# Optimization experiments

Measured on AMD Instinct MI355X. Metric: run time of the kernel, lower is better.

Reference implementation:

```python
import jax, jax.numpy as jnp
import numpy as np

N = 50000        # nodes
E = 1600000      # edges
NFEAT = 128      # node feature dim
NEDGE = 16       # raw edge feature dim
NHID = 128
NLAYER = 4
NGRAPH = 512
NOUT = 128
BN_EPS = 1e-5


def _bn(h, g, b):
    # eval-mode BatchNorm1d with running_mean=0, running_var=1
    return h * (g / jnp.sqrt(1.0 + BN_EPS)) + b


def setup_inputs() -> dict:
    key = jax.random.key(0)
    ks = jax.random.split(key, 24)
    s = 0.05
    inp = {
        "x": jax.random.normal(ks[0], (N, NFEAT), jnp.float32),
        "edge_index": jax.random.randint(ks[1], (2, E), 0, N, jnp.int64),
        "edge_attr": jax.random.normal(ks[2], (E, NEDGE), jnp.float32),
        "batch": jnp.sort(jax.random.randint(ks[3], (N,), 0, NGRAPH, jnp.int64)),
        # input encoder MLP (Linear + BN + ReLU)
        "in_W": jax.random.normal(ks[4], (NFEAT, NHID), jnp.float32) * s,
        "in_b": jnp.zeros((NHID,), jnp.float32),
        "in_g": jnp.ones((NHID,), jnp.float32),
        "in_beta": jnp.zeros((NHID,), jnp.float32),
        # per-layer edge encoder MLPs
        "edge_W": jax.random.normal(ks[5], (NLAYER, NEDGE, NHID), jnp.float32) * s,
        "edge_b": jnp.zeros((NLAYER, NHID), jnp.float32),
        "edge_g": jnp.ones((NLAYER, NHID), jnp.float32),
        "edge_beta": jnp.zeros((NLAYER, NHID), jnp.float32),
        # per-layer GINEConv linear (bias=False since bn=True) and eps
        "conv_W": jax.random.normal(ks[6], (NLAYER, NHID, NHID), jnp.float32) * s,
        "eps": jnp.zeros((NLAYER,), jnp.float32),
        # per-layer BatchNorm after conv
        "bn_g": jnp.ones((NLAYER, NHID), jnp.float32),
        "bn_b": jnp.zeros((NLAYER, NHID), jnp.float32),
        # output encoder: 2-layer MLP, norm after layer 1, no final activation
        "out_W1": jax.random.normal(ks[7], (NHID, NHID), jnp.float32) * s,
        "out_b1": jnp.zeros((NHID,), jnp.float32),
        "out_g1": jnp.ones((NHID,), jnp.float32),
        "out_beta1": jnp.zeros((NHID,), jnp.float32),
        "out_W2": jax.random.normal(ks[8], (NHID, NOUT), jnp.float32) * s,
        "out_b2": jnp.zeros((NOUT,), jnp.float32),
    }
    return inp


def reference(x, edge_index, edge_attr, batch,
              in_W, in_b, in_g, in_beta,
              edge_W, edge_b, edge_g, edge_beta,
              conv_W, eps, bn_g, bn_b,
              out_W1, out_b1, out_g1, out_beta1,
              out_W2, out_b2):
    # input encoder (MLP, 1 layer: Linear + BN + ReLU)
    h = jax.nn.relu(_bn(x @ in_W + in_b, in_g, in_beta))
    prev = h
    src, dst = edge_index[0], edge_index[1]
    for l in range(NLAYER):
        # edge encoder
        ea = jax.nn.relu(_bn(edge_attr @ edge_W[l] + edge_b[l], edge_g[l], edge_beta[l]))
        # GINEConv: messages relu(x_src + e), sum-aggregate to dst
        m = jax.nn.relu(h[src] + ea)                         # [E, NHID]
        agg = jax.ops.segment_sum(m, dst, num_segments=N)    # [N, NHID]
        h = ((1.0 + eps[l]) * h + agg) @ conv_W[l]
        h = jax.nn.relu(_bn(h, bn_g[l], bn_b[l]))            # dropout=0
        h = h + prev                                         # residual
        prev = h
    # add pooling over graphs
    pooled = jax.ops.segment_sum(h, batch, num_segments=NGRAPH)  # [NGRAPH, NHID]
    # output encoder: Linear+BN+ReLU, then Linear
    o = jax.nn.relu(_bn(pooled @ out_W1 + out_b1, out_g1, out_beta1))
    return o @ out_W2 + out_b2
```

## Files before the change

kernel.cpp:

```cpp
#include <hip/hip_runtime.h>
#include <stdint.h>

typedef uint32_t u32;
typedef _Float16 h2v __attribute__((ext_vector_type(2)));
typedef __attribute__((ext_vector_type(8))) short bf16x8;
typedef __attribute__((ext_vector_type(4))) float f32x4;

#define NGRAPH 512

__device__ __forceinline__ float uif(u32 u) { return __builtin_bit_cast(float, u); }
__device__ __forceinline__ u32 fiu(float f) { return __builtin_bit_cast(u32, f); }
__device__ __forceinline__ unsigned short bf16r(float f) {
    return (unsigned short)((fiu(f) + 0x8000u) >> 16);
}
__device__ __forceinline__ u32 pack_bf16(float lo, float hi) {
    return ((fiu(lo) + 0x8000u) >> 16) | ((fiu(hi) + 0x8000u) & 0xFFFF0000u);
}
__device__ __forceinline__ u32 pkh(float a, float b) {
    unsigned short la = __builtin_bit_cast(unsigned short, (_Float16)a);
    unsigned short hb = __builtin_bit_cast(unsigned short, (_Float16)b);
    return (u32)la | ((u32)hb << 16);
}
__device__ __forceinline__ float fdot2w(u32 a, u32 b, float c) {
#if __has_builtin(__builtin_amdgcn_fdot2)
    return __builtin_amdgcn_fdot2(__builtin_bit_cast(h2v, a),
                                  __builtin_bit_cast(h2v, b), c, false);
#else
    h2v av = __builtin_bit_cast(h2v, a), bv = __builtin_bit_cast(h2v, b);
    return c + (float)av[0]*(float)bv[0] + (float)av[1]*(float)bv[1];
#endif
}

__global__ __launch_bounds__(256) void prep_kernel(
    const float* __restrict__ in_b, const float* __restrict__ in_g, const float* __restrict__ in_beta,
    const float* __restrict__ edge_W,
    const float* __restrict__ edge_b, const float* __restrict__ edge_g, const float* __restrict__ edge_beta,
    const float* __restrict__ bn_g, const float* __restrict__ bn_b,
    const float* __restrict__ out_b1, const float* __restrict__ out_g1, const float* __restrict__ out_beta1,
    float* __restrict__ consts, u32* __restrict__ wpk)
{
    int c = threadIdx.x;
    if (c >= 128) return;
    const float rs = rsqrtf(1.0f + 1e-5f);
    float es = in_g[c] * rs;
    consts[c]       = es;
    consts[128 + c] = in_b[c] * es + in_beta[c];
    for (int l = 0; l < 4; ++l) {
        float s = edge_g[l*128 + c] * rs;
        consts[256  + l*128 + c] = s;
        consts[768  + l*128 + c] = edge_b[l*128 + c] * s + edge_beta[l*128 + c];
        float bs = bn_g[l*128 + c] * rs;
        consts[1280 + l*128 + c] = bs;
        consts[1792 + l*128 + c] = bn_b[l*128 + c];
        for (int kk = 0; kk < 8; ++kk) {
            float w0 = edge_W[(l*16 + 2*kk)*128 + c];
            float w1 = edge_W[(l*16 + 2*kk + 1)*128 + c];
            wpk[(l*8 + kk)*128 + c] = pkh(w0, w1);
        }
    }
    float s1 = out_g1[c] * rs;
    consts[2304 + c] = s1;
    consts[2432 + c] = out_b1[c] * s1 + out_beta1[c];
}

__global__ __launch_bounds__(256) void prepw_kernel(
    const float* __restrict__ in_W, const float* __restrict__ conv_W,
    unsigned short* __restrict__ WtAll)
{
    for (int idx = blockIdx.x*blockDim.x + threadIdx.x; idx < 5*128*128;
         idx += gridDim.x*blockDim.x) {
        int w = idx >> 14, rem = idx & 16383;
        int nn = rem >> 7, kk = rem & 127;
        const float* S = (w == 0) ? in_W : conv_W + (size_t)(w-1)*16384;
        WtAll[idx] = bf16r(S[kk*128 + nn]);
    }
}

__global__ __launch_bounds__(256) void xconv_kernel(
    const float* __restrict__ x, u32* __restrict__ x16, int n4)
{
    for (int i = blockIdx.x*blockDim.x + threadIdx.x; i < n4;
         i += gridDim.x*blockDim.x) {
        float4 v = *(const float4*)(x + (size_t)i*4);
        uint2 o; o.x = pack_bf16(v.x, v.y); o.y = pack_bf16(v.z, v.w);
        *(uint2*)(x16 + (size_t)i*2) = o;
    }
}

__global__ __launch_bounds__(256) void count_kernel(
    const int* __restrict__ dst, int E, int* __restrict__ cnt)
{
    for (int e = blockIdx.x*blockDim.x + threadIdx.x; e < E; e += gridDim.x*blockDim.x)
        atomicAdd(&cnt[dst[e]], 1);
}

__global__ __launch_bounds__(1024) void scan_kernel(
    const int* __restrict__ cnt, int n, int E,
    int* __restrict__ offs, int* __restrict__ cursor)
{
    __shared__ int sh[1024];
    const int t = threadIdx.x;
    const int chunk = (n + 1023) >> 10;
    const int lo = t * chunk;
    const int hi = min(n, lo + chunk);
    int s = 0;
    for (int i = lo; i < hi; ++i) s += cnt[i];
    sh[t] = s;
    __syncthreads();
    for (int d = 1; d < 1024; d <<= 1) {
        int v = (t >= d) ? sh[t - d] : 0;
        __syncthreads();
        sh[t] += v;
        __syncthreads();
    }
    int base = sh[t] - s;
    for (int i = lo; i < hi; ++i) { int c = cnt[i]; offs[i] = base; cursor[i] = base; base += c; }
    if (t == 1023) offs[n] = E;
}

__global__ __launch_bounds__(256) void scatter_kernel(
    const int* __restrict__ src, const int* __restrict__ dst,
    const float* __restrict__ attr, int E,
    int* __restrict__ cursor, int* __restrict__ srcoff, uint4* __restrict__ attrp)
{
    for (int e = blockIdx.x*blockDim.x + threadIdx.x; e < E; e += gridDim.x*blockDim.x) {
        int p = atomicAdd(&cursor[dst[e]], 1);
        srcoff[p] = src[e] * 256;
        const float4* ar = (const float4*)(attr + (size_t)e*16);
        float4 v0 = ar[0], v1 = ar[1], v2 = ar[2], v3 = ar[3];
        uint4 o0, o1;
        o0.x = pkh(v0.x, v0.y); o0.y = pkh(v0.z, v0.w);
        o0.z = pkh(v1.x, v1.y); o0.w = pkh(v1.z, v1.w);
        o1.x = pkh(v2.x, v2.y); o1.y = pkh(v2.z, v2.w);
        o1.z = pkh(v3.x, v3.y); o1.w = pkh(v3.z, v3.w);
        attrp[2*(size_t)p] = o0; attrp[2*(size_t)p + 1] = o1;
    }
}

__global__ __launch_bounds__(256) void goff_kernel(
    const int* __restrict__ batch, int n, int* __restrict__ goff)
{
    int g = blockIdx.x*blockDim.x + threadIdx.x;
    if (g > NGRAPH) return;
    if (g == NGRAPH) { goff[NGRAPH] = n; return; }
    int lo = 0, hi = n;
    while (lo < hi) { int m = (lo + hi) >> 1; if (batch[m] < g) lo = m + 1; else hi = m; }
    goff[g] = lo;
}

__global__ __launch_bounds__(256) void conv_mfma_kernel(
    const unsigned short* X16, int M,
    const unsigned short* __restrict__ Wt,
    const float* __restrict__ scale, const float* __restrict__ off,
    const unsigned short* __restrict__ resid16,
    unsigned short* out16, int do_relu)
{
    __shared__ unsigned short Ws[128*128];
    for (int i = threadIdx.x*8; i < 128*128; i += 256*8) {
        int row = i >> 7;
        int bo = (i & 127) * 2;
        int4 v = *(const int4*)(Wt + i);
        *(int4*)((char*)Ws + row*256 + (bo ^ ((row & 7) << 4))) = v;
    }
    __syncthreads();
    const int wave = threadIdx.x >> 6, lane = threadIdx.x & 63;
    const int row0 = blockIdx.x*64 + wave*16;
    const int l15 = lane & 15, l4 = lane >> 4;
    int arow = row0 + l15; if (arow > M-1) arow = M-1;
    const unsigned short* ap = X16 + (size_t)arow*128 + l4*8;
    f32x4 acc[8];
    #pragma unroll
    for (int t = 0; t < 8; ++t) acc[t] = f32x4{0.f, 0.f, 0.f, 0.f};
    #pragma unroll
    for (int ks = 0; ks < 4; ++ks) {
        bf16x8 a = *(const bf16x8*)(ap + ks*32);
        #pragma unroll
        for (int t = 0; t < 8; ++t) {
            int brow = t*16 + l15;
            int bo = ks*64 + l4*16;
            bf16x8 b = *(const bf16x8*)((const char*)Ws + brow*256 + (bo ^ ((brow & 7) << 4)));
            acc[t] = __builtin_amdgcn_mfma_f32_16x16x32_bf16(a, b, acc[t], 0, 0, 0);
        }
    }
    #pragma unroll
    for (int t = 0; t < 8; ++t) {
        int col = t*16 + l15;
        float sc = scale[col], of = off[col];
        #pragma unroll
        for (int r = 0; r < 4; ++r) {
            int row = row0 + l4*4 + r;
            if (row < M) {
                float y = fmaf(acc[t][r], sc, of);
                if (do_relu) y = fmaxf(y, 0.f);
                if (resid16) y += uif((u32)resid16[(size_t)row*128 + col] << 16);
                out16[(size_t)row*128 + col] = bf16r(y);
            }
        }
    }
}

__global__ __launch_bounds__(256) void agg_kernel(
    const char* __restrict__ hb,
    const uint4* __restrict__ attrp,
    const int* __restrict__ srcoff,
    const int* __restrict__ offs,
    const u32* __restrict__ wpk,
    const float* __restrict__ escale, const float* __restrict__ eoff,
    const float* __restrict__ epsp, int layer,
    u32* __restrict__ C16, int n)
{
    const int wave = threadIdx.x >> 6, lane = threadIdx.x & 63;
    const int lane4 = lane * 4;
    const int c0 = lane * 2;
    u32 wA[8], wB[8];
    #pragma unroll
    for (int kk = 0; kk < 8; ++kk) {
        wA[kk] = wpk[(layer*8 + kk)*128 + c0];
        wB[kk] = wpk[(layer*8 + kk)*128 + c0 + 1];
    }
    const float sc0 = escale[c0], sc1 = escale[c0+1];
    const float of0 = eoff[c0],   of1 = eoff[c0+1];
    const float epsv = 1.0f + epsp[layer];

    for (int node = blockIdx.x*4 + wave; node < n; node += gridDim.x*4) {
        const int beg = offs[node], end = offs[node+1];
        float acc0 = 0.f, acc1 = 0.f;

        auto edge = [&](int idx) {
            const int iu = __builtin_amdgcn_readfirstlane(idx);
            const uint4 q0 = attrp[2*(size_t)iu];
            const uint4 q1 = attrp[2*(size_t)iu + 1];
            const int so = srcoff[iu];
            const u32 hv = *(const u32*)(hb + so + lane4);
            float r0 = 0.f, r1 = 0.f;
            r0 = fdot2w(q0.x, wA[0], r0); r1 = fdot2w(q0.x, wB[0], r1);
            r0 = fdot2w(q0.y, wA[1], r0); r1 = fdot2w(q0.y, wB[1], r1);
            r0 = fdot2w(q0.z, wA[2], r0); r1 = fdot2w(q0.z, wB[2], r1);
            r0 = fdot2w(q0.w, wA[3], r0); r1 = fdot2w(q0.w, wB[3], r1);
            r0 = fdot2w(q1.x, wA[4], r0); r1 = fdot2w(q1.x, wB[4], r1);
            r0 = fdot2w(q1.y, wA[5], r0); r1 = fdot2w(q1.y, wB[5], r1);
            r0 = fdot2w(q1.z, wA[6], r0); r1 = fdot2w(q1.z, wB[6], r1);
            r0 = fdot2w(q1.w, wA[7], r0); r1 = fdot2w(q1.w, wB[7], r1);
            float ea0 = fmaxf(fmaf(r0, sc0, of0), 0.f);
            float ea1 = fmaxf(fmaf(r1, sc1, of1), 0.f);
            float h0 = uif(hv << 16);
            float h1 = uif(hv & 0xFFFF0000u);
            acc0 += fmaxf(h0 + ea0, 0.f);
            acc1 += fmaxf(h1 + ea1, 0.f);
        };

        int i = beg;
        for (; i + 1 < end; i += 2) { edge(i); edge(i + 1); }
        if (i < end) edge(i);

        const u32 hn = *(const u32*)(hb + (size_t)node*256 + lane4);
        float t0 = fmaf(epsv, uif(hn << 16), acc0);
        float t1 = fmaf(epsv, uif(hn & 0xFFFF0000u), acc1);
        C16[(size_t)node*64 + lane] = pack_bf16(t0, t1);
    }
}

__global__ __launch_bounds__(256) void pool_kernel(
    const u32* __restrict__ h16, const int* __restrict__ goff,
    float* __restrict__ pooled)
{
    const int wave = threadIdx.x >> 6, lane = threadIdx.x & 63;
    const int g = blockIdx.x*4 + wave;
    if (g >= NGRAPH) return;
    float ax = 0.f, ay = 0.f;
    const int beg = goff[g], end = goff[g+1];
    for (int node = beg; node < end; ++node) {
        u32 v = h16[(size_t)node*64 + lane];
        ax += uif(v << 16); ay += uif(v & 0xFFFF0000u);
    }
    *(float2*)&pooled[g*128 + lane*2] = make_float2(ax, ay);
}

__global__ __launch_bounds__(256) void gemm128_kernel(
    const float* __restrict__ in, int rows,
    const float* __restrict__ W,
    const float* __restrict__ scale, const float* __restrict__ off,
    float* out, int do_relu)
{
    __shared__ float Wsh[128*128];
    for (int i = threadIdx.x*4; i < 128*128; i += 256*4)
        *(float4*)&Wsh[i] = *(const float4*)&W[i];
    __syncthreads();
    const int wave = threadIdx.x >> 6, lane = threadIdx.x & 63;
    const int c0 = lane * 2;
    const float sc0 = scale ? scale[c0]   : 1.0f;
    const float sc1 = scale ? scale[c0+1] : 1.0f;
    const float of0 = off ? off[c0]   : 0.0f;
    const float of1 = off ? off[c0+1] : 0.0f;
    for (int rp = blockIdx.x*4 + wave; rp*2 < rows; rp += gridDim.x*4) {
        const int row0 = __builtin_amdgcn_readfirstlane(rp * 2);
        const float* xr = in + (size_t)row0 * 128;
        float a00 = 0.f, a01 = 0.f, a10 = 0.f, a11 = 0.f;
        #pragma unroll 8
        for (int k = 0; k < 128; ++k) {
            float x0 = xr[k];
            float x1 = xr[128 + k];
            float2 w = *(const float2*)&Wsh[k*128 + c0];
            a00 = fmaf(x0, w.x, a00); a01 = fmaf(x0, w.y, a01);
            a10 = fmaf(x1, w.x, a10); a11 = fmaf(x1, w.y, a11);
        }
        float y00 = fmaf(a00, sc0, of0), y01 = fmaf(a01, sc1, of1);
        float y10 = fmaf(a10, sc0, of0), y11 = fmaf(a11, sc1, of1);
        if (do_relu) {
            y00 = fmaxf(y00, 0.f); y01 = fmaxf(y01, 0.f);
            y10 = fmaxf(y10, 0.f); y11 = fmaxf(y11, 0.f);
        }
        *(float2*)&out[(size_t)row0*128 + c0]     = make_float2(y00, y01);
        *(float2*)&out[(size_t)(row0+1)*128 + c0] = make_float2(y10, y11);
    }
}

extern "C" void kernel_launch(void* const* d_in, const int* in_sizes, int n_in,
                              void* d_out, int out_size, void* d_ws, size_t ws_size,
                              hipStream_t stream)
{
    const float* x         = (const float*)d_in[0];
    const int*   eidx      = (const int*)d_in[1];
    const float* eattr     = (const float*)d_in[2];
    const int*   batch     = (const int*)d_in[3];
    const float* in_W      = (const float*)d_in[4];
    const float* in_b      = (const float*)d_in[5];
    const float* in_g      = (const float*)d_in[6];
    const float* in_beta   = (const float*)d_in[7];
    const float* edge_W    = (const float*)d_in[8];
    const float* edge_b    = (const float*)d_in[9];
    const float* edge_g    = (const float*)d_in[10];
    const float* edge_beta = (const float*)d_in[11];
    const float* conv_W    = (const float*)d_in[12];
    const float* epsp      = (const float*)d_in[13];
    const float* bn_g      = (const float*)d_in[14];
    const float* bn_b      = (const float*)d_in[15];
    const float* out_W1    = (const float*)d_in[16];
    const float* out_b1    = (const float*)d_in[17];
    const float* out_g1    = (const float*)d_in[18];
    const float* out_beta1 = (const float*)d_in[19];
    const float* out_W2    = (const float*)d_in[20];
    const float* out_b2    = (const float*)d_in[21];

    const int N = in_sizes[0] / 128;
    const int E = in_sizes[1] / 2;
    const int* src = eidx;
    const int* dst = eidx + E;

    char* ws = (char*)d_ws;
    size_t o = 0;
    auto alloc = [&](size_t bytes) { void* p = ws + o; o = (o + bytes + 255) & ~(size_t)255; return p; };
    unsigned short* P    = (unsigned short*)alloc((size_t)N * 128 * 2);
    unsigned short* Q    = (unsigned short*)alloc((size_t)N * 128 * 2);
    uint4* attrp         = (uint4*)alloc((size_t)E * 32);
    int*   srcoff        = (int*)alloc((size_t)E * 4);
    int*   offs          = (int*)alloc((size_t)(N + 1) * 4);
    int*   cursor        = (int*)alloc((size_t)N * 4);
    int*   cnt           = (int*)alloc((size_t)N * 4);
    int*   goff          = (int*)alloc((NGRAPH + 1) * 4);
    float* pooled        = (float*)alloc(NGRAPH * 128 * 4);
    float* o1            = (float*)alloc(NGRAPH * 128 * 4);
    float* consts        = (float*)alloc(2560 * 4);
    u32*   wpk           = (u32*)alloc(4 * 8 * 128 * 4);
    unsigned short* WtAll = (unsigned short*)alloc(5 * 128 * 128 * 2);

    prep_kernel<<<1, 256, 0, stream>>>(in_b, in_g, in_beta, edge_W,
                                       edge_b, edge_g, edge_beta,
                                       bn_g, bn_b, out_b1, out_g1, out_beta1,
                                       consts, wpk);
    prepw_kernel<<<80, 256, 0, stream>>>(in_W, conv_W, WtAll);
    xconv_kernel<<<2048, 256, 0, stream>>>(x, (u32*)Q, N * 32);

    (void)hipMemsetAsync(cnt, 0, (size_t)N * 4, stream);
    count_kernel<<<2048, 256, 0, stream>>>(dst, E, cnt);
    scan_kernel<<<1, 1024, 0, stream>>>(cnt, N, E, offs, cursor);
    scatter_kernel<<<2048, 256, 0, stream>>>(src, dst, eattr, E, cursor, srcoff, attrp);
    goff_kernel<<<3, 256, 0, stream>>>(batch, N, goff);

    const int gblocks = (N + 63) / 64;
    conv_mfma_kernel<<<gblocks, 256, 0, stream>>>(Q, N, WtAll,
                                                  consts, consts + 128,
                                                  nullptr, Q, 1);

    unsigned short* cur = Q;
    unsigned short* oth = P;
    for (int l = 0; l < 4; ++l) {
        agg_kernel<<<2048, 256, 0, stream>>>((const char*)cur, attrp, srcoff, offs,
                                             wpk,
                                             consts + 256 + l*128,
                                             consts + 768 + l*128,
                                             epsp, l, (u32*)oth, N);
        conv_mfma_kernel<<<gblocks, 256, 0, stream>>>(oth, N,
                                                      WtAll + (size_t)(1 + l)*16384,
                                                      consts + 1280 + l*128,
                                                      consts + 1792 + l*128,
                                                      cur, oth, 1);
        unsigned short* t = cur; cur = oth; oth = t;
    }

    pool_kernel<<<128, 256, 0, stream>>>((const u32*)cur, goff, pooled);

    gemm128_kernel<<<64, 256, 0, stream>>>(pooled, NGRAPH, out_W1,
                                           consts + 2304, consts + 2432, o1, 1);
    gemm128_kernel<<<64, 256, 0, stream>>>(o1, NGRAPH, out_W2,
                                           nullptr, out_b2, (float*)d_out, 0);
}
```

Before: 937.8 us.

## Software-pipeline edge loads in aggregation and double rows per MFMA block

The aggregation loop is rewritten to prefetch the next edge's attributes and source feature before computing the current edge, with a scheduling barrier to keep the loads ahead of the math. This hides gather latency along each node's edge list. The conv MFMA kernel now has each wave compute two 16-row tiles that share the same LDS weight reads, and the grid is halved. That amortizes the per-block weight staging into LDS but raises register use and leaves fewer blocks.

New measurement: 1.024 ms. +9.2%, slower.

```diff
diff --git a/kernel.cpp b/kernel.cpp
--- a/kernel.cpp
+++ b/kernel.cpp
@@ -164,22 +164,30 @@
     }
     __syncthreads();
     const int wave = threadIdx.x >> 6, lane = threadIdx.x & 63;
-    const int row0 = blockIdx.x*64 + wave*16;
     const int l15 = lane & 15, l4 = lane >> 4;
-    int arow = row0 + l15; if (arow > M-1) arow = M-1;
-    const unsigned short* ap = X16 + (size_t)arow*128 + l4*8;
-    f32x4 acc[8];
+    const int r0 = blockIdx.x*128 + wave*16;
+    const int r1 = r0 + 64;
+    const int ar0 = min(r0 + l15, M-1);
+    const int ar1 = min(r1 + l15, M-1);
+    const unsigned short* ap0 = X16 + (size_t)ar0*128 + l4*8;
+    const unsigned short* ap1 = X16 + (size_t)ar1*128 + l4*8;
+    f32x4 acc0[8], acc1[8];
     #pragma unroll
-    for (int t = 0; t < 8; ++t) acc[t] = f32x4{0.f, 0.f, 0.f, 0.f};
+    for (int t = 0; t < 8; ++t) {
+        acc0[t] = f32x4{0.f, 0.f, 0.f, 0.f};
+        acc1[t] = f32x4{0.f, 0.f, 0.f, 0.f};
+    }
     #pragma unroll
     for (int ks = 0; ks < 4; ++ks) {
-        bf16x8 a = *(const bf16x8*)(ap + ks*32);
+        bf16x8 a0 = *(const bf16x8*)(ap0 + ks*32);
+        bf16x8 a1 = *(const bf16x8*)(ap1 + ks*32);
         #pragma unroll
         for (int t = 0; t < 8; ++t) {
             int brow = t*16 + l15;
             int bo = ks*64 + l4*16;
             bf16x8 b = *(const bf16x8*)((const char*)Ws + brow*256 + (bo ^ ((brow & 7) << 4)));
-            acc[t] = __builtin_amdgcn_mfma_f32_16x16x32_bf16(a, b, acc[t], 0, 0, 0);
+            acc0[t] = __builtin_amdgcn_mfma_f32_16x16x32_bf16(a0, b, acc0[t], 0, 0, 0);
+            acc1[t] = __builtin_amdgcn_mfma_f32_16x16x32_bf16(a1, b, acc1[t], 0, 0, 0);
         }
     }
     #pragma unroll
@@ -188,15 +196,43 @@
         float sc = scale[col], of = off[col];
         #pragma unroll
         for (int r = 0; r < 4; ++r) {
-            int row = row0 + l4*4 + r;
+            int row = r0 + l4*4 + r;
             if (row < M) {
-                float y = fmaf(acc[t][r], sc, of);
+                float y = fmaf(acc0[t][r], sc, of);
                 if (do_relu) y = fmaxf(y, 0.f);
                 if (resid16) y += uif((u32)resid16[(size_t)row*128 + col] << 16);
                 out16[(size_t)row*128 + col] = bf16r(y);
             }
-        }
-    }
+            int row2 = r1 + l4*4 + r;
+            if (row2 < M) {
+                float y = fmaf(acc1[t][r], sc, of);
+                if (do_relu) y = fmaxf(y, 0.f);
+                if (resid16) y += uif((u32)resid16[(size_t)row2*128 + col] << 16);
+                out16[(size_t)row2*128 + col] = bf16r(y);
+            }
+        }
+    }
+}
+
+__device__ __forceinline__ void edge_math(
+    uint4 q0, uint4 q1, u32 hv,
+    const u32* wA, const u32* wB,
+    float sc0, float sc1, float of0, float of1,
+    float& acc0, float& acc1)
+{
+    float r0 = 0.f, r1 = 0.f;
+    r0 = fdot2w(q0.x, wA[0], r0); r1 = fdot2w(q0.x, wB[0], r1);
+    r0 = fdot2w(q0.y, wA[1], r0); r1 = fdot2w(q0.y, wB[1], r1);
+    r0 = fdot2w(q0.z, wA[2], r0); r1 = fdot2w(q0.z, wB[2], r1);
+    r0 = fdot2w(q0.w, wA[3], r0); r1 = fdot2w(q0.w, wB[3], r1);
+    r0 = fdot2w(q1.x, wA[4], r0); r1 = fdot2w(q1.x, wB[4], r1);
+    r0 = fdot2w(q1.y, wA[5], r0); r1 = fdot2w(q1.y, wB[5], r1);
+    r0 = fdot2w(q1.z, wA[6], r0); r1 = fdot2w(q1.z, wB[6], r1);
+    r0 = fdot2w(q1.w, wA[7], r0); r1 = fdot2w(q1.w, wB[7], r1);
+    float ea0 = fmaxf(fmaf(r0, sc0, of0), 0.f);
+    float ea1 = fmaxf(fmaf(r1, sc1, of1), 0.f);
+    acc0 += fmaxf(uif(hv << 16) + ea0, 0.f);
+    acc1 += fmaxf(uif(hv & 0xFFFF0000u) + ea1, 0.f);
 }
 
 __global__ __launch_bounds__(256) void agg_kernel(
@@ -225,34 +261,22 @@
     for (int node = blockIdx.x*4 + wave; node < n; node += gridDim.x*4) {
         const int beg = offs[node], end = offs[node+1];
         float acc0 = 0.f, acc1 = 0.f;
-
-        auto edge = [&](int idx) {
-            const int iu = __builtin_amdgcn_readfirstlane(idx);
-            const uint4 q0 = attrp[2*(size_t)iu];
-            const uint4 q1 = attrp[2*(size_t)iu + 1];
-            const int so = srcoff[iu];
-            const u32 hv = *(const u32*)(hb + so + lane4);
-            float r0 = 0.f, r1 = 0.f;
-            r0 = fdot2w(q0.x, wA[0], r0); r1 = fdot2w(q0.x, wB[0], r1);
-            r0 = fdot2w(q0.y, wA[1], r0); r1 = fdot2w(q0.y, wB[1], r1);
-            r0 = fdot2w(q0.z, wA[2], r0); r1 = fdot2w(q0.z, wB[2], r1);
-            r0 = fdot2w(q0.w, wA[3], r0); r1 = fdot2w(q0.w, wB[3], r1);
-            r0 = fdot2w(q1.x, wA[4], r0); r1 = fdot2w(q1.x, wB[4], r1);
-            r0 = fdot2w(q1.y, wA[5], r0); r1 = fdot2w(q1.y, wB[5], r1);
-            r0 = fdot2w(q1.z, wA[6], r0); r1 = fdot2w(q1.z, wB[6], r1);
-            r0 = fdot2w(q1.w, wA[7], r0); r1 = fdot2w(q1.w, wB[7], r1);
-            float ea0 = fmaxf(fmaf(r0, sc0, of0), 0.f);
-            float ea1 = fmaxf(fmaf(r1, sc1, of1), 0.f);
-            float h0 = uif(hv << 16);
-            float h1 = uif(hv & 0xFFFF0000u);
-            acc0 += fmaxf(h0 + ea0, 0.f);
-            acc1 += fmaxf(h1 + ea1, 0.f);
-        };
-
-        int i = beg;
-        for (; i + 1 < end; i += 2) { edge(i); edge(i + 1); }
-        if (i < end) edge(i);
-
+        if (beg < end) {
+            int iu = __builtin_amdgcn_readfirstlane(beg);
+            uint4 qA0 = attrp[2*(size_t)iu];
+            uint4 qA1 = attrp[2*(size_t)iu + 1];
+            u32 hvA = *(const u32*)(hb + srcoff[iu] + lane4);
+            for (int i = beg + 1; i < end; ++i) {
+                const int ju = __builtin_amdgcn_readfirstlane(i);
+                const uint4 qB0 = attrp[2*(size_t)ju];
+                const uint4 qB1 = attrp[2*(size_t)ju + 1];
+                const u32 hvB = *(const u32*)(hb + srcoff[ju] + lane4);
+                __builtin_amdgcn_sched_barrier(0);
+                edge_math(qA0, qA1, hvA, wA, wB, sc0, sc1, of0, of1, acc0, acc1);
+                qA0 = qB0; qA1 = qB1; hvA = hvB;
+            }
+            edge_math(qA0, qA1, hvA, wA, wB, sc0, sc1, of0, of1, acc0, acc1);
+        }
         const u32 hn = *(const u32*)(hb + (size_t)node*256 + lane4);
         float t0 = fmaf(epsv, uif(hn << 16), acc0);
         float t1 = fmaf(epsv, uif(hn & 0xFFFF0000u), acc1);
@@ -377,7 +401,7 @@
     scatter_kernel<<<2048, 256, 0, stream>>>(src, dst, eattr, E, cursor, srcoff, attrp);
     goff_kernel<<<3, 256, 0, stream>>>(batch, N, goff);
 
-    const int gblocks = (N + 63) / 64;
+    const int gblocks = (N + 127) / 128;
     conv_mfma_kernel<<<gblocks, 256, 0, stream>>>(Q, N, WtAll,
                                                   consts, consts + 128,
                                                   nullptr, Q, 1);
```

## Split edge-encoder aggregation from node gather and batch two layers per pass

Applied to the files above, without the earlier changes.

Since h and the encoded edge features are both non-negative, relu(h[src]+ea) equals h[src]+ea. The change therefore precomputes the per-node sum of relu-encoded edge features in a separate kernel that handles two layers per pass over the edge attributes. A lighter gather kernel then sums h[src] with four loads in flight and adds the precomputed edge sum. This halves edge-attribute reads and moves the dot-product work off the latency-bound gather path, at the cost of an extra 25 MB buffer and relying on the non-negativity invariant.

After: 991.0 us. 1.06x slower.

```diff
diff --git a/kernel.cpp b/kernel.cpp
--- a/kernel.cpp
+++ b/kernel.cpp
@@ -146,6 +146,99 @@
     int lo = 0, hi = n;
     while (lo < hi) { int m = (lo + hi) >> 1; if (batch[m] < g) lo = m + 1; else hi = m; }
     goff[g] = lo;
+}
+
+__global__ __launch_bounds__(256) void eagg2_kernel(
+    const uint4* __restrict__ attrp, const int* __restrict__ offs,
+    const u32* __restrict__ wpk, int lbase,
+    const float* __restrict__ consts,
+    u32* __restrict__ eagg, int n)
+{
+    const int wave = threadIdx.x >> 6, lane = threadIdx.x & 63;
+    const int c0 = lane * 2;
+    u32 wA0[8], wB0[8], wA1[8], wB1[8];
+    #pragma unroll
+    for (int kk = 0; kk < 8; ++kk) {
+        wA0[kk] = wpk[((lbase    )*8 + kk)*128 + c0];
+        wB0[kk] = wpk[((lbase    )*8 + kk)*128 + c0 + 1];
+        wA1[kk] = wpk[((lbase + 1)*8 + kk)*128 + c0];
+        wB1[kk] = wpk[((lbase + 1)*8 + kk)*128 + c0 + 1];
+    }
+    const float sA0 = consts[256 + lbase*128 + c0],     sA1 = consts[256 + lbase*128 + c0+1];
+    const float oA0 = consts[768 + lbase*128 + c0],     oA1 = consts[768 + lbase*128 + c0+1];
+    const float sB0 = consts[256 + (lbase+1)*128 + c0], sB1 = consts[256 + (lbase+1)*128 + c0+1];
+    const float oB0 = consts[768 + (lbase+1)*128 + c0], oB1 = consts[768 + (lbase+1)*128 + c0+1];
+
+    for (int node = blockIdx.x*4 + wave; node < n; node += gridDim.x*4) {
+        const int beg = offs[node], end = offs[node+1];
+        float a00 = 0.f, a01 = 0.f, a10 = 0.f, a11 = 0.f;
+        for (int i = beg; i < end; ++i) {
+            const int iu = __builtin_amdgcn_readfirstlane(i);
+            const uint4 q0 = attrp[2*(size_t)iu];
+            const uint4 q1 = attrp[2*(size_t)iu + 1];
+            float r0 = 0.f, r1 = 0.f, r2 = 0.f, r3 = 0.f;
+            r0 = fdot2w(q0.x, wA0[0], r0); r1 = fdot2w(q0.x, wB0[0], r1);
+            r2 = fdot2w(q0.x, wA1[0], r2); r3 = fdot2w(q0.x, wB1[0], r3);
+            r0 = fdot2w(q0.y, wA0[1], r0); r1 = fdot2w(q0.y, wB0[1], r1);
+            r2 = fdot2w(q0.y, wA1[1], r2); r3 = fdot2w(q0.y, wB1[1], r3);
+            r0 = fdot2w(q0.z, wA0[2], r0); r1 = fdot2w(q0.z, wB0[2], r1);
+            r2 = fdot2w(q0.z, wA1[2], r2); r3 = fdot2w(q0.z, wB1[2], r3);
+            r0 = fdot2w(q0.w, wA0[3], r0); r1 = fdot2w(q0.w, wB0[3], r1);
+            r2 = fdot2w(q0.w, wA1[3], r2); r3 = fdot2w(q0.w, wB1[3], r3);
+            r0 = fdot2w(q1.x, wA0[4], r0); r1 = fdot2w(q1.x, wB0[4], r1);
+            r2 = fdot2w(q1.x, wA1[4], r2); r3 = fdot2w(q1.x, wB1[4], r3);
+            r0 = fdot2w(q1.y, wA0[5], r0); r1 = fdot2w(q1.y, wB0[5], r1);
+            r2 = fdot2w(q1.y, wA1[5], r2); r3 = fdot2w(q1.y, wB1[5], r3);
+            r0 = fdot2w(q1.z, wA0[6], r0); r1 = fdot2w(q1.z, wB0[6], r1);
+            r2 = fdot2w(q1.z, wA1[6], r2); r3 = fdot2w(q1.z, wB1[6], r3);
+            r0 = fdot2w(q1.w, wA0[7], r0); r1 = fdot2w(q1.w, wB0[7], r1);
+            r2 = fdot2w(q1.w, wA1[7], r2); r3 = fdot2w(q1.w, wB1[7], r3);
+            a00 += fmaxf(fmaf(r0, sA0, oA0), 0.f);
+            a01 += fmaxf(fmaf(r1, sA1, oA1), 0.f);
+            a10 += fmaxf(fmaf(r2, sB0, oB0), 0.f);
+            a11 += fmaxf(fmaf(r3, sB1, oB1), 0.f);
+        }
+        eagg[(size_t)node*64 + lane]                 = pack_bf16(a00, a01);
+        eagg[(size_t)n*64 + (size_t)node*64 + lane]  = pack_bf16(a10, a11);
+    }
+}
+
+__global__ __launch_bounds__(256) void hagg_kernel(
+    const char* __restrict__ hb, const int* __restrict__ srcoff,
+    const int* __restrict__ offs, const u32* __restrict__ eagg_l,
+    const float* __restrict__ epsp, int layer,
+    u32* __restrict__ C16, int n)
+{
+    const int wave = threadIdx.x >> 6, lane = threadIdx.x & 63;
+    const int lane4 = lane * 4;
+    const float epsv = 1.0f + epsp[layer];
+    for (int node = blockIdx.x*4 + wave; node < n; node += gridDim.x*4) {
+        const int beg = offs[node], end = offs[node+1];
+        float acc0 = 0.f, acc1 = 0.f;
+        int i = beg;
+        for (; i + 3 < end; i += 4) {
+            const int iu = __builtin_amdgcn_readfirstlane(i);
+            const int4 so = *(const int4*)(srcoff + iu);
+            const u32 h0 = *(const u32*)(hb + so.x + lane4);
+            const u32 h1 = *(const u32*)(hb + so.y + lane4);
+            const u32 h2 = *(const u32*)(hb + so.z + lane4);
+            const u32 h3 = *(const u32*)(hb + so.w + lane4);
+            acc0 += uif(h0 << 16);          acc1 += uif(h0 & 0xFFFF0000u);
+            acc0 += uif(h1 << 16);          acc1 += uif(h1 & 0xFFFF0000u);
+            acc0 += uif(h2 << 16);          acc1 += uif(h2 & 0xFFFF0000u);
+            acc0 += uif(h3 << 16);          acc1 += uif(h3 & 0xFFFF0000u);
+        }
+        for (; i < end; ++i) {
+            const int iu = __builtin_amdgcn_readfirstlane(i);
+            const u32 h0 = *(const u32*)(hb + srcoff[iu] + lane4);
+            acc0 += uif(h0 << 16);          acc1 += uif(h0 & 0xFFFF0000u);
+        }
+        const u32 eg = eagg_l[(size_t)node*64 + lane];
+        const u32 hn = *(const u32*)(hb + (size_t)node*256 + lane4);
+        float t0 = fmaf(epsv, uif(hn << 16),          acc0 + uif(eg << 16));
+        float t1 = fmaf(epsv, uif(hn & 0xFFFF0000u),  acc1 + uif(eg & 0xFFFF0000u));
+        C16[(size_t)node*64 + lane] = pack_bf16(t0, t1);
+    }
 }
 
 __global__ __launch_bounds__(256) void conv_mfma_kernel(
@@ -196,67 +289,6 @@
                 out16[(size_t)row*128 + col] = bf16r(y);
             }
         }
-    }
-}
-
-__global__ __launch_bounds__(256) void agg_kernel(
-    const char* __restrict__ hb,
-    const uint4* __restrict__ attrp,
-    const int* __restrict__ srcoff,
-    const int* __restrict__ offs,
-    const u32* __restrict__ wpk,
-    const float* __restrict__ escale, const float* __restrict__ eoff,
-    const float* __restrict__ epsp, int layer,
-    u32* __restrict__ C16, int n)
-{
-    const int wave = threadIdx.x >> 6, lane = threadIdx.x & 63;
-    const int lane4 = lane * 4;
-    const int c0 = lane * 2;
-    u32 wA[8], wB[8];
-    #pragma unroll
-    for (int kk = 0; kk < 8; ++kk) {
-        wA[kk] = wpk[(layer*8 + kk)*128 + c0];
-        wB[kk] = wpk[(layer*8 + kk)*128 + c0 + 1];
-    }
-    const float sc0 = escale[c0], sc1 = escale[c0+1];
-    const float of0 = eoff[c0],   of1 = eoff[c0+1];
-    const float epsv = 1.0f + epsp[layer];
-
-    for (int node = blockIdx.x*4 + wave; node < n; node += gridDim.x*4) {
-        const int beg = offs[node], end = offs[node+1];
-        float acc0 = 0.f, acc1 = 0.f;
-
-        auto edge = [&](int idx) {
-            const int iu = __builtin_amdgcn_readfirstlane(idx);
-            const uint4 q0 = attrp[2*(size_t)iu];
-            const uint4 q1 = attrp[2*(size_t)iu + 1];
-            const int so = srcoff[iu];
-            const u32 hv = *(const u32*)(hb + so + lane4);
-            float r0 = 0.f, r1 = 0.f;
-            r0 = fdot2w(q0.x, wA[0], r0); r1 = fdot2w(q0.x, wB[0], r1);
-            r0 = fdot2w(q0.y, wA[1], r0); r1 = fdot2w(q0.y, wB[1], r1);
-            r0 = fdot2w(q0.z, wA[2], r0); r1 = fdot2w(q0.z, wB[2], r1);
-            r0 = fdot2w(q0.w, wA[3], r0); r1 = fdot2w(q0.w, wB[3], r1);
-            r0 = fdot2w(q1.x, wA[4], r0); r1 = fdot2w(q1.x, wB[4], r1);
-            r0 = fdot2w(q1.y, wA[5], r0); r1 = fdot2w(q1.y, wB[5], r1);
-            r0 = fdot2w(q1.z, wA[6], r0); r1 = fdot2w(q1.z, wB[6], r1);
-            r0 = fdot2w(q1.w, wA[7], r0); r1 = fdot2w(q1.w, wB[7], r1);
-            float ea0 = fmaxf(fmaf(r0, sc0, of0), 0.f);
-            float ea1 = fmaxf(fmaf(r1, sc1, of1), 0.f);
-            float h0 = uif(hv << 16);
-            float h1 = uif(hv & 0xFFFF0000u);
-            acc0 += fmaxf(h0 + ea0, 0.f);
-            acc1 += fmaxf(h1 + ea1, 0.f);
-        };
-
-        int i = beg;
-        for (; i + 1 < end; i += 2) { edge(i); edge(i + 1); }
-        if (i < end) edge(i);
-
-        const u32 hn = *(const u32*)(hb + (size_t)node*256 + lane4);
-        float t0 = fmaf(epsv, uif(hn << 16), acc0);
-        float t1 = fmaf(epsv, uif(hn & 0xFFFF0000u), acc1);
-        C16[(size_t)node*64 + lane] = pack_bf16(t0, t1);
     }
 }
 
@@ -354,6 +386,7 @@
     unsigned short* Q    = (unsigned short*)alloc((size_t)N * 128 * 2);
     uint4* attrp         = (uint4*)alloc((size_t)E * 32);
     int*   srcoff        = (int*)alloc((size_t)E * 4);
+    u32*   eagg          = (u32*)alloc((size_t)N * 64 * 2 * 4);
     int*   offs          = (int*)alloc((size_t)(N + 1) * 4);
     int*   cursor        = (int*)alloc((size_t)N * 4);
     int*   cnt           = (int*)alloc((size_t)N * 4);
@@ -381,15 +414,16 @@
     conv_mfma_kernel<<<gblocks, 256, 0, stream>>>(Q, N, WtAll,
                                                   consts, consts + 128,
                                                   nullptr, Q, 1);
+    eagg2_kernel<<<2048, 256, 0, stream>>>(attrp, offs, wpk, 0, consts, eagg, N);
 
     unsigned short* cur = Q;
     unsigned short* oth = P;
     for (int l = 0; l < 4; ++l) {
-        agg_kernel<<<2048, 256, 0, stream>>>((const char*)cur, attrp, srcoff, offs,
-                                             wpk,
-                                             consts + 256 + l*128,
-                                             consts + 768 + l*128,
-                                             epsp, l, (u32*)oth, N);
+        if (l == 2)
+            eagg2_kernel<<<2048, 256, 0, stream>>>(attrp, offs, wpk, 2, consts, eagg, N);
+        hagg_kernel<<<2048, 256, 0, stream>>>((const char*)cur, srcoff, offs,
+                                              eagg + (size_t)(l & 1) * N * 64,
+                                              epsp, l, (u32*)oth, N);
         conv_mfma_kernel<<<gblocks, 256, 0, stream>>>(oth, N,
                                                       WtAll + (size_t)(1 + l)*16384,
                                                       consts + 1280 + l*128,
```
